# Kernel optimization log

Hardware: AMD Instinct MI355X
Metric: run time of the kernel (lower is better)

The kernel has to match this reference:

```python
import jax, jax.numpy as jnp
import numpy as np

N = 2097152   # total points across all samples
B = 8         # number of point clouds in the batch
C = 64        # feature channels of fea


def setup_inputs() -> dict:
    key = jax.random.key(0)
    k1, k2, k3, k4 = jax.random.split(key, 4)
    fea = jax.random.normal(k1, (N, C), dtype=jnp.float32)
    pred_f = jax.random.normal(k2, (N, 1), dtype=jnp.float32)
    batch_ids = jnp.sort(jax.random.randint(k3, (N,), 0, B).astype(jnp.int32))
    target_points_num = jax.random.randint(k4, (B,), 0, 250000).astype(jnp.int32)
    return {"fea": fea, "pred_f": pred_f, "batch_ids": batch_ids,
            "target_points_num": target_points_num}


def reference(fea, pred_f, batch_ids, target_points_num):
    """BCE branch of GenerativeUpsample.get_keep + feature pruning.

    For each sample b with n_b points and target t_b: if n_b > t_b, threshold is the
    (n_b - t_b)-th smallest pred value (torch.kthvalue, 1-indexed), else dtype min.
    keep = pred > threshold[batch_id]; pruned fea = fea masked by keep.
    """
    vals = pred_f[:, 0]                                  # [N]
    n = vals.shape[0]
    counts = jax.ops.segment_sum(jnp.ones((n,), jnp.int32), batch_ids,
                                 num_segments=B)         # [B] points per sample
    offsets = jnp.concatenate([jnp.zeros((1,), jnp.int32),
                               jnp.cumsum(counts)[:-1].astype(jnp.int32)])
    pos = jnp.arange(n, dtype=jnp.int32) - offsets[batch_ids]  # index within segment

    # Pad each sample's values into a dense row (pad=+inf so pads sort to the end).
    dense = jnp.full((B, n), jnp.inf, dtype=vals.dtype).at[batch_ids, pos].set(vals)
    dense_sorted = jnp.sort(dense, axis=1)               # [B, N]

    # kth smallest (1-indexed k = n_b - t_b) -> sorted index n_b - t_b - 1.
    k_idx = jnp.clip(counts - target_points_num - 1, 0, n - 1)
    kth = jnp.take_along_axis(dense_sorted, k_idx[:, None].astype(jnp.int32), axis=1)[:, 0]
    thresh = jnp.where(counts > target_points_num, kth,
                       jnp.finfo(vals.dtype).min)        # [B]

    keep = vals > thresh[batch_ids]                      # [N] bool
    pruned_fea = fea * keep[:, None].astype(fea.dtype)   # [N, C]
    return pruned_fea, keep
```

## Files before the change

kernel.cpp:

```cpp
#include <hip/hip_runtime.h>
#include <float.h>


#define BATCHES 8

__device__ __forceinline__ unsigned f2key(float x) {
    unsigned u = __float_as_uint(x);
    return (u & 0x80000000u) ? ~u : (u | 0x80000000u);
}
__device__ __forceinline__ float key2f(unsigned k) {
    unsigned u = (k & 0x80000000u) ? (k & 0x7FFFFFFFu) : ~k;
    return __uint_as_float(u);
}

static constexpr int HIST_OFF   = 0;
static constexpr int COUNTS_OFF = 8192;
static constexpr int REMK_OFF   = 8200;
static constexpr int PREFIX_OFF = 8208;
static constexpr int ACTIVE_OFF = 8216;
static constexpr int THRESH_OFF = 8224;
static constexpr int WS_INTS    = 8232;

__global__ __launch_bounds__(256) void hist0_kernel(const float* __restrict__ pred,
                                                    const int* __restrict__ bids,
                                                    unsigned* __restrict__ hist,
                                                    int n) {
    __shared__ unsigned lh[BATCHES * 256];
    for (int i = threadIdx.x; i < BATCHES * 256; i += blockDim.x) lh[i] = 0u;
    __syncthreads();
    int stride = gridDim.x * blockDim.x;
    for (int i = blockIdx.x * blockDim.x + threadIdx.x; i < n; i += stride) {
        int b = bids[i];
        unsigned key = f2key(pred[i]);
        atomicAdd(&lh[b * 256 + (key >> 24)], 1u);
    }
    __syncthreads();
    for (int i = threadIdx.x; i < BATCHES * 256; i += blockDim.x) {
        unsigned v = lh[i];
        if (v) atomicAdd(&hist[i], v);
    }
}

__global__ void scan0_kernel(const unsigned* __restrict__ hist,
                             const int* __restrict__ target,
                             unsigned* __restrict__ counts,
                             unsigned* __restrict__ remk,
                             unsigned* __restrict__ prefix,
                             unsigned* __restrict__ active) {
    int b = threadIdx.x;
    if (b >= BATCHES) return;
    const unsigned* h = hist + b * 256;
    unsigned total = 0;
    for (int i = 0; i < 256; i++) total += h[i];
    counts[b] = total;
    int t = target[b];
    if ((int)total > t && total > 0) {
        unsigned r = total - (unsigned)t - 1u;
        unsigned cum = 0;
        int bin = 255;
        for (int i = 0; i < 256; i++) {
            unsigned c = h[i];
            if (cum + c > r) { bin = i; break; }
            cum += c;
        }
        prefix[b] = (unsigned)bin;
        remk[b] = r - cum;
        active[b] = 1u;
    } else {
        active[b] = 0u;
    }
}

__global__ __launch_bounds__(256) void histN_kernel(const float* __restrict__ pred,
                                                    const int* __restrict__ bids,
                                                    const unsigned* __restrict__ prefix,
                                                    const unsigned* __restrict__ active,
                                                    unsigned* __restrict__ hist,
                                                    int n, int shiftHi, int shiftBin) {
    int i = blockIdx.x * blockDim.x + threadIdx.x;
    if (i >= n) return;
    int b = bids[i];
    if (!active[b]) return;
    unsigned key = f2key(pred[i]);
    if ((key >> shiftHi) == prefix[b])
        atomicAdd(&hist[b * 256 + ((key >> shiftBin) & 0xFFu)], 1u);
}

__global__ void scanN_kernel(const unsigned* __restrict__ hist,
                             unsigned* __restrict__ remk,
                             unsigned* __restrict__ prefix,
                             const unsigned* __restrict__ active,
                             float* __restrict__ thresh,
                             int finalize) {
    int b = threadIdx.x;
    if (b >= BATCHES) return;
    if (active[b]) {
        const unsigned* h = hist + b * 256;
        unsigned r = remk[b];
        unsigned cum = 0;
        int bin = 255;
        for (int i = 0; i < 256; i++) {
            unsigned c = h[i];
            if (cum + c > r) { bin = i; break; }
            cum += c;
        }
        prefix[b] = (prefix[b] << 8) | (unsigned)bin;
        remk[b] = r - cum;
        if (finalize) thresh[b] = key2f(prefix[b]);
    } else {
        if (finalize) thresh[b] = -FLT_MAX;
    }
}

__global__ __launch_bounds__(256) void prune_kernel(const float* __restrict__ fea,
                                                    const float* __restrict__ pred,
                                                    const int* __restrict__ bids,
                                                    const float* __restrict__ thresh,
                                                    float* __restrict__ out,
                                                    int n) {
    int idx = blockIdx.x * blockDim.x + threadIdx.x;
    int row = idx >> 4;
    int l = idx & 15;
    if (row >= n) return;
    int b = bids[row];
    bool kp = pred[row] > thresh[b];
    float4* dst = (float4*)out + (size_t)row * 16 + l;
    if (kp) {
        *dst = ((const float4*)fea)[(size_t)row * 16 + l];
    } else {
        *dst = make_float4(0.f, 0.f, 0.f, 0.f);
    }
    if (l == 0) out[(size_t)n * 64 + row] = kp ? 1.0f : 0.0f;
}

extern "C" void kernel_launch(void* const* d_in, const int* in_sizes, int n_in,
                              void* d_out, int out_size, void* d_ws, size_t ws_size,
                              hipStream_t stream) {
    const float* fea    = (const float*)d_in[0];
    const float* pred   = (const float*)d_in[1];
    const int*   bids   = (const int*)d_in[2];
    const int*   target = (const int*)d_in[3];
    float* out = (float*)d_out;
    int n = in_sizes[1];

    unsigned* ws      = (unsigned*)d_ws;
    unsigned* hist    = ws + HIST_OFF;
    unsigned* counts  = ws + COUNTS_OFF;
    unsigned* remk    = ws + REMK_OFF;
    unsigned* prefix  = ws + PREFIX_OFF;
    unsigned* active  = ws + ACTIVE_OFF;
    float*    thresh  = (float*)(ws + THRESH_OFF);

    hipMemsetAsync(d_ws, 0, WS_INTS * sizeof(unsigned), stream);

    hist0_kernel<<<1024, 256, 0, stream>>>(pred, bids, hist, n);
    scan0_kernel<<<1, 64, 0, stream>>>(hist, target, counts, remk, prefix, active);

    int nblk = (n + 255) / 256;
    for (int p = 1; p <= 3; p++) {
        unsigned* hp = hist + p * BATCHES * 256;
        int shiftHi = 32 - 8 * p;
        int shiftBin = 24 - 8 * p;
        histN_kernel<<<nblk, 256, 0, stream>>>(pred, bids, prefix, active, hp, n,
                                               shiftHi, shiftBin);
        scanN_kernel<<<1, 64, 0, stream>>>(hp, remk, prefix, active, thresh,
                                           p == 3 ? 1 : 0);
    }

    long total4 = (long)n * 16;
    int pblk = (int)((total4 + 255) / 256);
    prune_kernel<<<pblk, 256, 0, stream>>>(fea, pred, bids, thresh, out, n);
}
```

Before: 1.071 ms.

## Use LDS-privatized radix histograms, parallel block scans, and grid-stride prune

```diff
diff --git a/kernel.cpp b/kernel.cpp
--- a/kernel.cpp
+++ b/kernel.cpp
@@ -14,12 +14,11 @@
 }
 
 static constexpr int HIST_OFF   = 0;
-static constexpr int COUNTS_OFF = 8192;
-static constexpr int REMK_OFF   = 8200;
-static constexpr int PREFIX_OFF = 8208;
-static constexpr int ACTIVE_OFF = 8216;
-static constexpr int THRESH_OFF = 8224;
-static constexpr int WS_INTS    = 8232;
+static constexpr int REMK_OFF   = 8192;
+static constexpr int PREFIX_OFF = 8200;
+static constexpr int ACTIVE_OFF = 8208;
+static constexpr int THRESH_OFF = 8216;
+static constexpr int WS_INTS    = 8224;
 
 __global__ __launch_bounds__(256) void hist0_kernel(const float* __restrict__ pred,
                                                     const int* __restrict__ bids,
@@ -41,74 +40,80 @@
     }
 }
 
-__global__ void scan0_kernel(const unsigned* __restrict__ hist,
-                             const int* __restrict__ target,
-                             unsigned* __restrict__ counts,
-                             unsigned* __restrict__ remk,
-                             unsigned* __restrict__ prefix,
-                             unsigned* __restrict__ active) {
-    int b = threadIdx.x;
-    if (b >= BATCHES) return;
-    const unsigned* h = hist + b * 256;
-    unsigned total = 0;
-    for (int i = 0; i < 256; i++) total += h[i];
-    counts[b] = total;
-    int t = target[b];
-    if ((int)total > t && total > 0) {
-        unsigned r = total - (unsigned)t - 1u;
-        unsigned cum = 0;
-        int bin = 255;
-        for (int i = 0; i < 256; i++) {
-            unsigned c = h[i];
-            if (cum + c > r) { bin = i; break; }
-            cum += c;
-        }
-        prefix[b] = (unsigned)bin;
-        remk[b] = r - cum;
-        active[b] = 1u;
-    } else {
-        active[b] = 0u;
-    }
-}
-
 __global__ __launch_bounds__(256) void histN_kernel(const float* __restrict__ pred,
                                                     const int* __restrict__ bids,
                                                     const unsigned* __restrict__ prefix,
                                                     const unsigned* __restrict__ active,
                                                     unsigned* __restrict__ hist,
                                                     int n, int shiftHi, int shiftBin) {
-    int i = blockIdx.x * blockDim.x + threadIdx.x;
-    if (i >= n) return;
-    int b = bids[i];
-    if (!active[b]) return;
-    unsigned key = f2key(pred[i]);
-    if ((key >> shiftHi) == prefix[b])
-        atomicAdd(&hist[b * 256 + ((key >> shiftBin) & 0xFFu)], 1u);
+    __shared__ unsigned lh[BATCHES * 256];
+    __shared__ unsigned lpre[BATCHES];
+    __shared__ unsigned lact[BATCHES];
+    for (int i = threadIdx.x; i < BATCHES * 256; i += blockDim.x) lh[i] = 0u;
+    if (threadIdx.x < BATCHES) {
+        lpre[threadIdx.x] = prefix[threadIdx.x];
+        lact[threadIdx.x] = active[threadIdx.x];
+    }
+    __syncthreads();
+    int stride = gridDim.x * blockDim.x;
+    for (int i = blockIdx.x * blockDim.x + threadIdx.x; i < n; i += stride) {
+        int b = bids[i];
+        if (!lact[b]) continue;
+        unsigned key = f2key(pred[i]);
+        if ((key >> shiftHi) == lpre[b])
+            atomicAdd(&lh[b * 256 + ((key >> shiftBin) & 0xFFu)], 1u);
+    }
+    __syncthreads();
+    for (int i = threadIdx.x; i < BATCHES * 256; i += blockDim.x) {
+        unsigned v = lh[i];
+        if (v) atomicAdd(&hist[i], v);
+    }
 }
 
-__global__ void scanN_kernel(const unsigned* __restrict__ hist,
-                             unsigned* __restrict__ remk,
-                             unsigned* __restrict__ prefix,
-                             const unsigned* __restrict__ active,
-                             float* __restrict__ thresh,
-                             int finalize) {
-    int b = threadIdx.x;
-    if (b >= BATCHES) return;
-    if (active[b]) {
-        const unsigned* h = hist + b * 256;
-        unsigned r = remk[b];
-        unsigned cum = 0;
-        int bin = 255;
-        for (int i = 0; i < 256; i++) {
-            unsigned c = h[i];
-            if (cum + c > r) { bin = i; break; }
-            cum += c;
-        }
-        prefix[b] = (prefix[b] << 8) | (unsigned)bin;
-        remk[b] = r - cum;
-        if (finalize) thresh[b] = key2f(prefix[b]);
+__global__ __launch_bounds__(256) void scan_kernel(const unsigned* __restrict__ hist,
+                                                   const int* __restrict__ target,
+                                                   unsigned* __restrict__ remk,
+                                                   unsigned* __restrict__ prefix,
+                                                   unsigned* __restrict__ active,
+                                                   float* __restrict__ thresh,
+                                                   int pass) {
+    int b = blockIdx.x;
+    int t = threadIdx.x;
+    if (pass > 0 && !active[b]) {
+        if (pass == 3 && t == 0) thresh[b] = -FLT_MAX;
+        return;
+    }
+    __shared__ unsigned s[256];
+    const unsigned* h = hist + (pass * BATCHES + b) * 256;
+    unsigned c = h[t];
+    s[t] = c;
+    __syncthreads();
+    for (int off = 1; off < 256; off <<= 1) {
+        unsigned v = s[t];
+        unsigned a = (t >= off) ? s[t - off] : 0u;
+        __syncthreads();
+        s[t] = v + a;
+        __syncthreads();
+    }
+    unsigned incl = s[t];
+    unsigned total = s[255];
+    unsigned r;
+    if (pass == 0) {
+        int tg = target[b];
+        bool act = ((int)total > tg) && (total > 0u);
+        if (t == 0) active[b] = act ? 1u : 0u;
+        if (!act) return;
+        r = total - (unsigned)tg - 1u;
     } else {
-        if (finalize) thresh[b] = -FLT_MAX;
+        r = remk[b];
+    }
+    __syncthreads();
+    unsigned excl = incl - c;
+    if (c > 0u && excl <= r && r < incl) {
+        unsigned p = (pass == 0) ? (unsigned)t : ((prefix[b] << 8) | (unsigned)t);
+        prefix[b] = p;
+        remk[b] = r - excl;
+        if (pass == 3) thresh[b] = key2f(p);
     }
 }
 
@@ -118,19 +123,25 @@
                                                     const float* __restrict__ thresh,
                                                     float* __restrict__ out,
                                                     int n) {
-    int idx = blockIdx.x * blockDim.x + threadIdx.x;
-    int row = idx >> 4;
-    int l = idx & 15;
-    if (row >= n) return;
-    int b = bids[row];
-    bool kp = pred[row] > thresh[b];
-    float4* dst = (float4*)out + (size_t)row * 16 + l;
-    if (kp) {
-        *dst = ((const float4*)fea)[(size_t)row * 16 + l];
-    } else {
-        *dst = make_float4(0.f, 0.f, 0.f, 0.f);
+    __shared__ float sth[BATCHES];
+    if (threadIdx.x < BATCHES) sth[threadIdx.x] = thresh[threadIdx.x];
+    __syncthreads();
+    long total4 = (long)n * 16;
+    long stride = (long)gridDim.x * blockDim.x;
+    for (long idx = (long)blockIdx.x * blockDim.x + threadIdx.x; idx < total4;
+         idx += stride) {
+        int row = (int)(idx >> 4);
+        int l = (int)(idx & 15);
+        int b = bids[row];
+        bool kp = pred[row] > sth[b];
+        float4* dst = (float4*)out + idx;
+        if (kp) {
+            *dst = ((const float4*)fea)[idx];
+        } else {
+            *dst = make_float4(0.f, 0.f, 0.f, 0.f);
+        }
+        if (l == 0) out[(size_t)n * 64 + row] = kp ? 1.0f : 0.0f;
     }
-    if (l == 0) out[(size_t)n * 64 + row] = kp ? 1.0f : 0.0f;
 }
 
 extern "C" void kernel_launch(void* const* d_in, const int* in_sizes, int n_in,
@@ -145,29 +156,26 @@
 
     unsigned* ws      = (unsigned*)d_ws;
     unsigned* hist    = ws + HIST_OFF;
-    unsigned* counts  = ws + COUNTS_OFF;
     unsigned* remk    = ws + REMK_OFF;
     unsigned* prefix  = ws + PREFIX_OFF;
     unsigned* active  = ws + ACTIVE_OFF;
     float*    thresh  = (float*)(ws + THRESH_OFF);
 
-    hipMemsetAsync(d_ws, 0, WS_INTS * sizeof(unsigned), stream);
+    hipMemsetAsync(hist, 0, 4 * BATCHES * 256 * sizeof(unsigned), stream);
 
     hist0_kernel<<<1024, 256, 0, stream>>>(pred, bids, hist, n);
-    scan0_kernel<<<1, 64, 0, stream>>>(hist, target, counts, remk, prefix, active);
+    scan_kernel<<<BATCHES, 256, 0, stream>>>(hist, target, remk, prefix, active,
+                                             thresh, 0);
 
-    int nblk = (n + 255) / 256;
     for (int p = 1; p <= 3; p++) {
         unsigned* hp = hist + p * BATCHES * 256;
         int shiftHi = 32 - 8 * p;
         int shiftBin = 24 - 8 * p;
-        histN_kernel<<<nblk, 256, 0, stream>>>(pred, bids, prefix, active, hp, n,
+        histN_kernel<<<2048, 256, 0, stream>>>(pred, bids, prefix, active, hp, n,
                                                shiftHi, shiftBin);
-        scanN_kernel<<<1, 64, 0, stream>>>(hp, remk, prefix, active, thresh,
-                                           p == 3 ? 1 : 0);
+        scan_kernel<<<BATCHES, 256, 0, stream>>>(hist, target, remk, prefix, active,
+                                                 thresh, p);
     }
 
-    long total4 = (long)n * 16;
-    int pblk = (int)((total4 + 255) / 256);
-    prune_kernel<<<pblk, 256, 0, stream>>>(fea, pred, bids, thresh, out, n);
+    prune_kernel<<<8192, 256, 0, stream>>>(fea, pred, bids, thresh, out, n);
 }
```

Result: faster. 899.6 us (-16.0%).
